# Optimization experiments

Hardware: AMD Instinct MI355X
Metric: run time of the kernel (lower is better)

Reference implementation:

```python
import jax, jax.numpy as jnp
import numpy as np

BLOCK_H = 32  # block_h from init
BLOCK_W = 32  # block_w from init


def _block_pool(mask, bh, bw):
    # mask: [H, S, S] int -> block mask [H, S//bh, S//bw] bool
    # Equivalent to the grouped Conv2d with all-ones kernel, stride=(bh,bw), then >0.
    H, S1, S2 = mask.shape
    m = mask.reshape(H, S1 // bh, bh, S2 // bw, bw).astype(jnp.float32)
    return m.sum(axis=(2, 4)) > 0


def _expand_block_mask(bm, bh, bw):
    # bm: [H, Nb_r, Nb_c] bool -> element mask [H, S, S] bool
    H, nr, nc = bm.shape
    e = jnp.broadcast_to(bm[:, :, None, :, None], (H, nr, bh, nc, bw))
    return e.reshape(H, nr * bh, nc * bw)


def setup_inputs() -> dict:
    key = jax.random.key(0)
    kq, kk, kv, km = jax.random.split(key, 4)
    Z, H, S, D = 1, 16, 2048, 64
    query = jax.random.normal(kq, (Z, H, S, D), dtype=jnp.float32)
    key_t = jax.random.normal(kk, (Z, H, S, D), dtype=jnp.float32)
    value = jax.random.normal(kv, (Z, H, S, D), dtype=jnp.float32)
    mask = jax.random.randint(km, (H, S, S), 0, 2, dtype=jnp.int32)
    return {"query": query, "key": key_t, "value": value, "mask": mask}


def reference(query, key, value, mask):
    # Dense equivalent of: sdd QK^T on layout blocks -> blocksparse causal
    # softmax (scale=1.0) -> dsd AV. Rows with no active blocks yield zeros,
    # matching the blocksparse representation (absent blocks contribute 0).
    H, S, _ = mask.shape
    bm = _block_pool(mask, BLOCK_H, BLOCK_W)              # [H, Nb, Nb]
    elem = _expand_block_mask(bm, BLOCK_H, BLOCK_W)       # [H, S, S]
    causal = jnp.tril(jnp.ones((S, S), dtype=bool))       # is_causal=True
    full = elem & causal                                  # [H, S, S]
    scale = 1.0                                           # scale=1.0 in forward

    scores = jnp.einsum('zhqd,zhkd->zhqk', query, key) * scale
    neg = jnp.asarray(-1e30, dtype=scores.dtype)
    scores = jnp.where(full[None], scores, neg)
    probs = jax.nn.softmax(scores, axis=-1)
    row_valid = jnp.any(full, axis=-1)                    # [H, S]
    probs = jnp.where(row_valid[None, :, :, None], probs, 0.0)
    out = jnp.einsum('zhqk,zhkd->zhqd', probs, value)
    return out
```

## Files before the change

kernel.cpp:

```cpp
#include <hip/hip_runtime.h>
#include <stdint.h>


#define HH 16
#define SS 2048
#define DD 64

using f32x4  = __attribute__((ext_vector_type(4))) float;
using s16x8  = __attribute__((ext_vector_type(8))) short;
using s16x4  = __attribute__((ext_vector_type(4))) short;
using bf16x8 = __attribute__((ext_vector_type(8))) __bf16;

#define AS1 __attribute__((address_space(1)))
#define AS3 __attribute__((address_space(3)))

__device__ __forceinline__ unsigned short f2bf(float f) {
  unsigned u = __builtin_bit_cast(unsigned, f);
  u += 0x7fffu + ((u >> 16) & 1u);
  return (unsigned short)(u >> 16);
}
__device__ __forceinline__ float bf2f(unsigned short u) {
  return __builtin_bit_cast(float, ((unsigned)u) << 16);
}

template <int CTRL>
__device__ __forceinline__ float dpp_step(float x) {
  int y = __builtin_amdgcn_update_dpp(__builtin_bit_cast(int, x),
                                      __builtin_bit_cast(int, x),
                                      CTRL, 0xF, 0xF, false);
  return __builtin_bit_cast(float, y);
}
__device__ __forceinline__ float row16_sum(float x) {
  x += dpp_step<0xB1>(x);
  x += dpp_step<0x4E>(x);
  x += dpp_step<0x141>(x);
  x += dpp_step<0x140>(x);
  return x;
}

__global__ __launch_bounds__(256) void prep_kernel(
    const int* __restrict__ mask, const float* __restrict__ K,
    const float* __restrict__ V, unsigned char* __restrict__ bmask,
    unsigned short* __restrict__ Khi, unsigned short* __restrict__ Klo,
    unsigned short* __restrict__ Vtb) {
  __shared__ float tile[64][65];
  const int wg = blockIdx.x;
  const int t  = threadIdx.x;
  if (wg < 256) {
    const int tid = wg * 256 + t;
    {
      const int h = tid >> 12, br = (tid >> 6) & 63, bc = tid & 63;
      const int4* p = (const int4*)(mask + ((size_t)(h * SS + br * 32) * SS + bc * 32));
      int acc = 0;
#pragma unroll
      for (int i = 0; i < 8; ++i) { int4 v = p[i]; acc |= v.x | v.y | v.z | v.w; }
      if (acc == 0) {
        for (int r = 1; r < 32; ++r) {
          const int4* q2 = (const int4*)(mask + ((size_t)(h * SS + br * 32 + r) * SS + bc * 32));
          int a2 = 0;
#pragma unroll
          for (int i = 0; i < 8; ++i) { int4 v = q2[i]; a2 |= v.x | v.y | v.z | v.w; }
          acc |= a2;
          if (acc) break;
        }
      }
      bmask[tid] = acc != 0 ? 1 : 0;
    }
    {
      const float4* K4 = (const float4*)K;
      ushort4* Kh4 = (ushort4*)Khi;
      ushort4* Kl4 = (ushort4*)Klo;
#pragma unroll
      for (int i = 0; i < 8; ++i) {
        float4 v = K4[(size_t)i * 65536 + tid];
        ushort4 hi, lo;
        hi.x = f2bf(v.x); lo.x = f2bf(v.x - bf2f(hi.x));
        hi.y = f2bf(v.y); lo.y = f2bf(v.y - bf2f(hi.y));
        hi.z = f2bf(v.z); lo.z = f2bf(v.z - bf2f(hi.z));
        hi.w = f2bf(v.w); lo.w = f2bf(v.w - bf2f(hi.w));
        Kh4[(size_t)i * 65536 + tid] = hi;
        Kl4[(size_t)i * 65536 + tid] = lo;
      }
    }
  } else {
    const int w2 = wg - 256;
    const int h = w2 >> 5, kt = w2 & 31;
    const float4* V4 = (const float4*)V;
#pragma unroll
    for (int j2 = 0; j2 < 4; ++j2) {
      int fi = t + j2 * 256;
      int row = fi >> 4, c4 = (fi & 15) * 4;
      float4 v = V4[(size_t)(h * SS + kt * 64 + row) * 16 + (fi & 15)];
      tile[row][c4] = v.x; tile[row][c4+1] = v.y; tile[row][c4+2] = v.z; tile[row][c4+3] = v.w;
    }
    __syncthreads();
    const int d = t >> 2, ks = (t & 3) * 16;
#pragma unroll
    for (int c = 0; c < 4; ++c) {
      ushort4 o;
      o.x = f2bf(tile[ks + c*4 + 0][d]);
      o.y = f2bf(tile[ks + c*4 + 1][d]);
      o.z = f2bf(tile[ks + c*4 + 2][d]);
      o.w = f2bf(tile[ks + c*4 + 3][d]);
      ((ushort4*)Vtb)[((size_t)(h * 64 + d) * SS + kt * 64 + ks + c*4) >> 2] = o;
    }
  }
}

__global__ __launch_bounds__(256, 1) void attn_kernel(
    const float* __restrict__ Q, const unsigned char* __restrict__ bmask,
    const unsigned short* __restrict__ Khi, const unsigned short* __restrict__ Klo,
    const unsigned short* __restrict__ Vtb, float* __restrict__ O) {
  const int id = blockIdx.x;
  const int h  = id & 15;
  const int p  = id >> 4;

  const int t    = threadIdx.x;
  const int wave = t >> 6, lane = t & 63;
  const int n16  = lane & 15, quad = lane >> 4;

  __shared__ __align__(16) short ldsKV[24576];
  __shared__ __align__(16) short ldsP[4][1088];

  const unsigned short* gk[2]; const unsigned short* gl[2]; const unsigned short* gv[2];
  int lofs[2];
#pragma unroll
  for (int i = 0; i < 2; ++i) {
    int slot = i * 256 + t;
    int row  = slot >> 3;
    int c8   = (slot & 7) ^ (row & 7);
    lofs[i] = slot * 8;
    gk[i] = Khi + (size_t)h * SS * DD + row * DD + c8 * 8;
    gl[i] = Klo + (size_t)h * SS * DD + row * DD + c8 * 8;
    gv[i] = Vtb + ((size_t)(h * 64 + row)) * SS + c8 * 8;
  }
  auto stage = [&](int kt, int buf) {
    short* kb = ldsKV + buf * 12288;
#pragma unroll
    for (int i = 0; i < 2; ++i) {
      __builtin_amdgcn_global_load_lds((const AS1 void*)(gk[i] + kt * 4096),
                                       (AS3 void*)(kb + lofs[i]), 16, 0, 0);
      __builtin_amdgcn_global_load_lds((const AS1 void*)(gl[i] + kt * 4096),
                                       (AS3 void*)(kb + 4096 + lofs[i]), 16, 0, 0);
      __builtin_amdgcn_global_load_lds((const AS1 void*)(gv[i] + kt * 64),
                                       (AS3 void*)(kb + 8192 + lofs[i]), 16, 0, 0);
    }
  };

  s16x8 qhi[2], qlo[2];
  auto load_q = [&](int qb) {
    const float* qp = Q + ((size_t)(h * SS + qb * 64 + wave * 16 + n16)) * DD + quad * 8;
#pragma unroll
    for (int kc = 0; kc < 2; ++kc) {
      float4 a = *(const float4*)(qp + kc * 32);
      float4 b = *(const float4*)(qp + kc * 32 + 4);
      float x[8] = {a.x, a.y, a.z, a.w, b.x, b.y, b.z, b.w};
      s16x8 fh, fl;
#pragma unroll
      for (int e = 0; e < 8; ++e) {
        unsigned short hi = f2bf(x[e]);
        fh[e] = (short)hi;
        fl[e] = (short)f2bf(x[e] - bf2f(hi));
      }
      qhi[kc] = fh; qlo[kc] = fl;
    }
  };
  auto load_bmw = [&](int qb) {
    int qbr = qb * 2 + (wave >> 1);
    return __ballot(bmask[(h << 12) + (qbr << 6) + lane] != 0);
  };

  float l_i[4];
  f32x4 oa[4];
  auto reset_state = [&]() {
#pragma unroll
    for (int r = 0; r < 4; ++r) l_i[r] = 0.f;
#pragma unroll
    for (int db = 0; db < 4; ++db) oa[db] = f32x4{0.f, 0.f, 0.f, 0.f};
  };
  auto store_o = [&](int qb) {
    float* op = O + ((size_t)(h * SS + qb * 64 + wave * 16)) * DD;
#pragma unroll
    for (int r = 0; r < 4; ++r) {
      int qrow = quad * 4 + r;
      float lsum = row16_sum(l_i[r]);
      float inv = lsum > 0.f ? 1.f / lsum : 0.f;
#pragma unroll
      for (int db = 0; db < 4; ++db) {
        op[(size_t)qrow * DD + db * 16 + n16] = oa[db][r] * inv;
      }
    }
  };

  int qb = p, qi0 = p * 64 + wave * 16;
  load_q(p);
  unsigned long long bmw = load_bmw(p);
  reset_state();
  stage(0, 0);

  for (int s = 0; s < 33; ++s) {
    __syncthreads();
    const int kt = (s <= p) ? s : s - p - 1;
    if (s < 32) {
      int s2 = s + 1;
      stage((s2 <= p) ? s2 : s2 - p - 1, s2 & 1);
    }
    if (s == p + 1) {
      store_o(p);
      qb = 31 - p; qi0 = qb * 64 + wave * 16;
      load_q(qb); bmw = load_bmw(qb);
      reset_state();
    }

    const short* khb = ldsKV + (s & 1) * 12288;
    const short* klb = khb + 4096;
    const short* vbase = khb + 8192;

    f32x4 S[4];
#pragma unroll
    for (int nb = 0; nb < 4; ++nb) S[nb] = f32x4{0.f, 0.f, 0.f, 0.f};
#pragma unroll
    for (int kc = 0; kc < 2; ++kc) {
      bf16x8 ah = __builtin_bit_cast(bf16x8, qhi[kc]);
      bf16x8 al8 = __builtin_bit_cast(bf16x8, qlo[kc]);
#pragma unroll
      for (int nb = 0; nb < 4; ++nb) {
        int row = nb * 16 + n16;
        int pc  = (kc * 4 + quad) ^ (row & 7);
        bf16x8 kh = __builtin_bit_cast(bf16x8, *(const s16x8*)(khb + row * 64 + pc * 8));
        bf16x8 kl = __builtin_bit_cast(bf16x8, *(const s16x8*)(klb + row * 64 + pc * 8));
        S[nb] = __builtin_amdgcn_mfma_f32_16x16x32_bf16(ah, kh, S[nb], 0, 0, 0);
        S[nb] = __builtin_amdgcn_mfma_f32_16x16x32_bf16(al8, kh, S[nb], 0, 0, 0);
        S[nb] = __builtin_amdgcn_mfma_f32_16x16x32_bf16(ah, kl, S[nb], 0, 0, 0);
      }
    }

    const int b0 = (int)((bmw >> (kt * 2)) & 1ull);
    const int b1 = (int)((bmw >> (kt * 2 + 1)) & 1ull);
    if ((kt == qb) | !(b0 & b1)) {
#pragma unroll
      for (int nb = 0; nb < 4; ++nb) {
        int kj = kt * 64 + nb * 16 + n16;
        int bb = (nb < 2) ? b0 : b1;
#pragma unroll
        for (int r = 0; r < 4; ++r) {
          int qi = qi0 + quad * 4 + r;
          bool ok = (kj <= qi) && (bb != 0);
          S[nb][r] = ok ? S[nb][r] : -__builtin_inff();
        }
      }
    }

#pragma unroll
    for (int nb = 0; nb < 4; ++nb) {
#pragma unroll
      for (int r = 0; r < 4; ++r) {
        float pv = __expf(S[nb][r]);
        unsigned short pq = f2bf(pv);
        ldsP[wave][(quad * 4 + r) * 68 + nb * 16 + n16] = (short)pq;
        l_i[r] += bf2f(pq);
      }
    }

#pragma unroll
    for (int kc = 0; kc < 2; ++kc) {
      const short* pp = &ldsP[wave][n16 * 68 + kc * 32 + quad * 8];
      s16x4 x = *(const s16x4*)pp;
      s16x4 y = *(const s16x4*)(pp + 4);
      s16x8 pf8 = {x[0], x[1], x[2], x[3], y[0], y[1], y[2], y[3]};
      bf16x8 ap = __builtin_bit_cast(bf16x8, pf8);
#pragma unroll
      for (int db = 0; db < 4; ++db) {
        int row = db * 16 + n16;
        int pc  = (kc * 4 + quad) ^ (n16 & 7);
        s16x8 vv = *(const s16x8*)(vbase + row * 64 + pc * 8);
        oa[db] = __builtin_amdgcn_mfma_f32_16x16x32_bf16(
            ap, __builtin_bit_cast(bf16x8, vv), oa[db], 0, 0, 0);
      }
    }
  }

  store_o(31 - p);
}

extern "C" void kernel_launch(void* const* d_in, const int* in_sizes, int n_in,
                              void* d_out, int out_size, void* d_ws, size_t ws_size,
                              hipStream_t stream) {
  const float* Q   = (const float*)d_in[0];
  const float* K   = (const float*)d_in[1];
  const float* V   = (const float*)d_in[2];
  const int* mask  = (const int*)d_in[3];
  float* out       = (float*)d_out;

  unsigned char* bmask = (unsigned char*)d_ws;
  unsigned short* Khi  = (unsigned short*)((char*)d_ws + 65536);
  unsigned short* Klo  = (unsigned short*)((char*)d_ws + 65536 + 4194304);
  unsigned short* Vtb  = (unsigned short*)((char*)d_ws + 65536 + 2 * 4194304);

  prep_kernel<<<768, 256, 0, stream>>>(mask, K, V, bmask, Khi, Klo, Vtb);
  attn_kernel<<<256, 256, 0, stream>>>(Q, bmask, Khi, Klo, Vtb, out);
}
```

Measured before the change: 355.8 us.

## Process both paired query blocks concurrently with 8 waves sharing K/V tiles

Each block now runs 512 threads: waves 0-3 handle query block p and waves 4-7 handle query block 31-p. Both groups read the same staged K/V tile, so tiles 0..p are loaded once instead of twice. Before, one set of waves walked the two query blocks one after the other. Each thread stages one 16-byte chunk per tensor instead of two. The loop runs up to 31-p tiles, and waves for the short block sit idle on later tiles while still waiting at the barriers. This raises per-block occupancy but brings wave imbalance within the block.

```diff
diff --git a/kernel.cpp b/kernel.cpp
--- a/kernel.cpp
+++ b/kernel.cpp
@@ -107,7 +107,7 @@
   }
 }
 
-__global__ __launch_bounds__(256, 1) void attn_kernel(
+__global__ __launch_bounds__(512, 1) void attn_kernel(
     const float* __restrict__ Q, const unsigned char* __restrict__ bmask,
     const unsigned short* __restrict__ Khi, const unsigned short* __restrict__ Klo,
     const unsigned short* __restrict__ Vtb, float* __restrict__ O) {
@@ -118,38 +118,33 @@
   const int t    = threadIdx.x;
   const int wave = t >> 6, lane = t & 63;
   const int n16  = lane & 15, quad = lane >> 4;
+  const int wsub = wave & 3;
+  const int qb   = (wave < 4) ? p : (31 - p);
+  const int lastkt = 31 - p;
 
   __shared__ __align__(16) short ldsKV[24576];
-  __shared__ __align__(16) short ldsP[4][1088];
-
-  const unsigned short* gk[2]; const unsigned short* gl[2]; const unsigned short* gv[2];
-  int lofs[2];
-#pragma unroll
-  for (int i = 0; i < 2; ++i) {
-    int slot = i * 256 + t;
-    int row  = slot >> 3;
-    int c8   = (slot & 7) ^ (row & 7);
-    lofs[i] = slot * 8;
-    gk[i] = Khi + (size_t)h * SS * DD + row * DD + c8 * 8;
-    gl[i] = Klo + (size_t)h * SS * DD + row * DD + c8 * 8;
-    gv[i] = Vtb + ((size_t)(h * 64 + row)) * SS + c8 * 8;
-  }
+  __shared__ __align__(16) short ldsP[8][1088];
+
+  const int srow = t >> 3;
+  const int c8   = (t & 7) ^ (srow & 7);
+  const unsigned short* gk = Khi + (size_t)h * SS * DD + srow * DD + c8 * 8;
+  const unsigned short* gl = Klo + (size_t)h * SS * DD + srow * DD + c8 * 8;
+  const unsigned short* gv = Vtb + ((size_t)(h * 64 + srow)) * SS + c8 * 8;
+  const int lofs = t * 8;
   auto stage = [&](int kt, int buf) {
     short* kb = ldsKV + buf * 12288;
-#pragma unroll
-    for (int i = 0; i < 2; ++i) {
-      __builtin_amdgcn_global_load_lds((const AS1 void*)(gk[i] + kt * 4096),
-                                       (AS3 void*)(kb + lofs[i]), 16, 0, 0);
-      __builtin_amdgcn_global_load_lds((const AS1 void*)(gl[i] + kt * 4096),
-                                       (AS3 void*)(kb + 4096 + lofs[i]), 16, 0, 0);
-      __builtin_amdgcn_global_load_lds((const AS1 void*)(gv[i] + kt * 64),
-                                       (AS3 void*)(kb + 8192 + lofs[i]), 16, 0, 0);
-    }
+    __builtin_amdgcn_global_load_lds((const AS1 void*)(gk + kt * 4096),
+                                     (AS3 void*)(kb + lofs), 16, 0, 0);
+    __builtin_amdgcn_global_load_lds((const AS1 void*)(gl + kt * 4096),
+                                     (AS3 void*)(kb + 4096 + lofs), 16, 0, 0);
+    __builtin_amdgcn_global_load_lds((const AS1 void*)(gv + kt * 64),
+                                     (AS3 void*)(kb + 8192 + lofs), 16, 0, 0);
   };
 
+  const int qi0 = qb * 64 + wsub * 16;
   s16x8 qhi[2], qlo[2];
-  auto load_q = [&](int qb) {
-    const float* qp = Q + ((size_t)(h * SS + qb * 64 + wave * 16 + n16)) * DD + quad * 8;
+  {
+    const float* qp = Q + ((size_t)(h * SS + qi0 + n16)) * DD + quad * 8;
 #pragma unroll
     for (int kc = 0; kc < 2; ++kc) {
       float4 a = *(const float4*)(qp + kc * 32);
@@ -164,22 +159,95 @@
       }
       qhi[kc] = fh; qlo[kc] = fl;
     }
-  };
-  auto load_bmw = [&](int qb) {
-    int qbr = qb * 2 + (wave >> 1);
-    return __ballot(bmask[(h << 12) + (qbr << 6) + lane] != 0);
-  };
+  }
+
+  const int qbr = qb * 2 + (wsub >> 1);
+  const unsigned long long bmw = __ballot(bmask[(h << 12) + (qbr << 6) + lane] != 0);
 
   float l_i[4];
   f32x4 oa[4];
-  auto reset_state = [&]() {
-#pragma unroll
-    for (int r = 0; r < 4; ++r) l_i[r] = 0.f;
-#pragma unroll
-    for (int db = 0; db < 4; ++db) oa[db] = f32x4{0.f, 0.f, 0.f, 0.f};
-  };
-  auto store_o = [&](int qb) {
-    float* op = O + ((size_t)(h * SS + qb * 64 + wave * 16)) * DD;
+#pragma unroll
+  for (int r = 0; r < 4; ++r) l_i[r] = 0.f;
+#pragma unroll
+  for (int db = 0; db < 4; ++db) oa[db] = f32x4{0.f, 0.f, 0.f, 0.f};
+
+  stage(0, 0);
+  for (int kt = 0; kt <= lastkt; ++kt) {
+    __syncthreads();
+    if (kt < lastkt) stage(kt + 1, (kt + 1) & 1);
+
+    if (kt <= qb) {
+      const short* khb = ldsKV + (kt & 1) * 12288;
+      const short* klb = khb + 4096;
+      const short* vbase = khb + 8192;
+
+      f32x4 S[4];
+#pragma unroll
+      for (int nb = 0; nb < 4; ++nb) S[nb] = f32x4{0.f, 0.f, 0.f, 0.f};
+#pragma unroll
+      for (int kc = 0; kc < 2; ++kc) {
+        bf16x8 ah = __builtin_bit_cast(bf16x8, qhi[kc]);
+        bf16x8 al8 = __builtin_bit_cast(bf16x8, qlo[kc]);
+#pragma unroll
+        for (int nb = 0; nb < 4; ++nb) {
+          int row = nb * 16 + n16;
+          int pc  = (kc * 4 + quad) ^ (row & 7);
+          bf16x8 kh = __builtin_bit_cast(bf16x8, *(const s16x8*)(khb + row * 64 + pc * 8));
+          bf16x8 kl = __builtin_bit_cast(bf16x8, *(const s16x8*)(klb + row * 64 + pc * 8));
+          S[nb] = __builtin_amdgcn_mfma_f32_16x16x32_bf16(ah, kh, S[nb], 0, 0, 0);
+          S[nb] = __builtin_amdgcn_mfma_f32_16x16x32_bf16(al8, kh, S[nb], 0, 0, 0);
+          S[nb] = __builtin_amdgcn_mfma_f32_16x16x32_bf16(ah, kl, S[nb], 0, 0, 0);
+        }
+      }
+
+      const int b0 = (int)((bmw >> (kt * 2)) & 1ull);
+      const int b1 = (int)((bmw >> (kt * 2 + 1)) & 1ull);
+      if ((kt == qb) | !(b0 & b1)) {
+#pragma unroll
+        for (int nb = 0; nb < 4; ++nb) {
+          int kj = kt * 64 + nb * 16 + n16;
+          int bb = (nb < 2) ? b0 : b1;
+#pragma unroll
+          for (int r = 0; r < 4; ++r) {
+            int qi = qi0 + quad * 4 + r;
+            bool ok = (kj <= qi) && (bb != 0);
+            S[nb][r] = ok ? S[nb][r] : -__builtin_inff();
+          }
+        }
+      }
+
+#pragma unroll
+      for (int nb = 0; nb < 4; ++nb) {
+#pragma unroll
+        for (int r = 0; r < 4; ++r) {
+          float pv = __expf(S[nb][r]);
+          unsigned short pq = f2bf(pv);
+          ldsP[wave][(quad * 4 + r) * 68 + nb * 16 + n16] = (short)pq;
+          l_i[r] += bf2f(pq);
+        }
+      }
+
+#pragma unroll
+      for (int kc = 0; kc < 2; ++kc) {
+        const short* pp = &ldsP[wave][n16 * 68 + kc * 32 + quad * 8];
+        s16x4 x = *(const s16x4*)pp;
+        s16x4 y = *(const s16x4*)(pp + 4);
+        s16x8 pf8 = {x[0], x[1], x[2], x[3], y[0], y[1], y[2], y[3]};
+        bf16x8 ap = __builtin_bit_cast(bf16x8, pf8);
+#pragma unroll
+        for (int db = 0; db < 4; ++db) {
+          int row = db * 16 + n16;
+          int pc  = (kc * 4 + quad) ^ (n16 & 7);
+          s16x8 vv = *(const s16x8*)(vbase + row * 64 + pc * 8);
+          oa[db] = __builtin_amdgcn_mfma_f32_16x16x32_bf16(
+              ap, __builtin_bit_cast(bf16x8, vv), oa[db], 0, 0, 0);
+        }
+      }
+    }
+  }
+
+  {
+    float* op = O + ((size_t)(h * SS + qi0)) * DD;
 #pragma unroll
     for (int r = 0; r < 4; ++r) {
       int qrow = quad * 4 + r;
@@ -190,97 +258,7 @@
         op[(size_t)qrow * DD + db * 16 + n16] = oa[db][r] * inv;
       }
     }
-  };
-
-  int qb = p, qi0 = p * 64 + wave * 16;
-  load_q(p);
-  unsigned long long bmw = load_bmw(p);
-  reset_state();
-  stage(0, 0);
-
-  for (int s = 0; s < 33; ++s) {
-    __syncthreads();
-    const int kt = (s <= p) ? s : s - p - 1;
-    if (s < 32) {
-      int s2 = s + 1;
-      stage((s2 <= p) ? s2 : s2 - p - 1, s2 & 1);
-    }
-    if (s == p + 1) {
-      store_o(p);
-      qb = 31 - p; qi0 = qb * 64 + wave * 16;
-      load_q(qb); bmw = load_bmw(qb);
-      reset_state();
-    }
-
-    const short* khb = ldsKV + (s & 1) * 12288;
-    const short* klb = khb + 4096;
-    const short* vbase = khb + 8192;
-
-    f32x4 S[4];
-#pragma unroll
-    for (int nb = 0; nb < 4; ++nb) S[nb] = f32x4{0.f, 0.f, 0.f, 0.f};
-#pragma unroll
-    for (int kc = 0; kc < 2; ++kc) {
-      bf16x8 ah = __builtin_bit_cast(bf16x8, qhi[kc]);
-      bf16x8 al8 = __builtin_bit_cast(bf16x8, qlo[kc]);
-#pragma unroll
-      for (int nb = 0; nb < 4; ++nb) {
-        int row = nb * 16 + n16;
-        int pc  = (kc * 4 + quad) ^ (row & 7);
-        bf16x8 kh = __builtin_bit_cast(bf16x8, *(const s16x8*)(khb + row * 64 + pc * 8));
-        bf16x8 kl = __builtin_bit_cast(bf16x8, *(const s16x8*)(klb + row * 64 + pc * 8));
-        S[nb] = __builtin_amdgcn_mfma_f32_16x16x32_bf16(ah, kh, S[nb], 0, 0, 0);
-        S[nb] = __builtin_amdgcn_mfma_f32_16x16x32_bf16(al8, kh, S[nb], 0, 0, 0);
-        S[nb] = __builtin_amdgcn_mfma_f32_16x16x32_bf16(ah, kl, S[nb], 0, 0, 0);
-      }
-    }
-
-    const int b0 = (int)((bmw >> (kt * 2)) & 1ull);
-    const int b1 = (int)((bmw >> (kt * 2 + 1)) & 1ull);
-    if ((kt == qb) | !(b0 & b1)) {
-#pragma unroll
-      for (int nb = 0; nb < 4; ++nb) {
-        int kj = kt * 64 + nb * 16 + n16;
-        int bb = (nb < 2) ? b0 : b1;
-#pragma unroll
-        for (int r = 0; r < 4; ++r) {
-          int qi = qi0 + quad * 4 + r;
-          bool ok = (kj <= qi) && (bb != 0);
-          S[nb][r] = ok ? S[nb][r] : -__builtin_inff();
-        }
-      }
-    }
-
-#pragma unroll
-    for (int nb = 0; nb < 4; ++nb) {
-#pragma unroll
-      for (int r = 0; r < 4; ++r) {
-        float pv = __expf(S[nb][r]);
-        unsigned short pq = f2bf(pv);
-        ldsP[wave][(quad * 4 + r) * 68 + nb * 16 + n16] = (short)pq;
-        l_i[r] += bf2f(pq);
-      }
-    }
-
-#pragma unroll
-    for (int kc = 0; kc < 2; ++kc) {
-      const short* pp = &ldsP[wave][n16 * 68 + kc * 32 + quad * 8];
-      s16x4 x = *(const s16x4*)pp;
-      s16x4 y = *(const s16x4*)(pp + 4);
-      s16x8 pf8 = {x[0], x[1], x[2], x[3], y[0], y[1], y[2], y[3]};
-      bf16x8 ap = __builtin_bit_cast(bf16x8, pf8);
-#pragma unroll
-      for (int db = 0; db < 4; ++db) {
-        int row = db * 16 + n16;
-        int pc  = (kc * 4 + quad) ^ (n16 & 7);
-        s16x8 vv = *(const s16x8*)(vbase + row * 64 + pc * 8);
-        oa[db] = __builtin_amdgcn_mfma_f32_16x16x32_bf16(
-            ap, __builtin_bit_cast(bf16x8, vv), oa[db], 0, 0, 0);
-      }
-    }
-  }
-
-  store_o(31 - p);
+  }
 }
 
 extern "C" void kernel_launch(void* const* d_in, const int* in_sizes, int n_in,
@@ -298,5 +276,5 @@
   unsigned short* Vtb  = (unsigned short*)((char*)d_ws + 65536 + 2 * 4194304);
 
   prep_kernel<<<768, 256, 0, stream>>>(mask, K, V, bmask, Khi, Klo, Vtb);
-  attn_kernel<<<256, 256, 0, stream>>>(Q, bmask, Khi, Klo, Vtb, out);
-}
+  attn_kernel<<<256, 512, 0, stream>>>(Q, bmask, Khi, Klo, Vtb, out);
+}
```

Measured after the change: 360.3 us. No clear change (+1.3%).
